# Kernel optimization log

Measured on AMD Instinct MI355X. Metric: run time of the kernel, lower is better.

## Reference

```python
import jax, jax.numpy as jnp
import numpy as np

N = 8192      # nodes
E = 16384     # query edges
D = 256       # node feature dim
NNZ = 262144  # overlap matrix nnz (avg degree 32)
P1, P2, P3 = 32, 32, 32


def _mlp(x, W1, b1, W2, b2):
    # Linear(1->p) -> ReLU -> Linear(p->1)
    return jax.nn.relu(x @ W1 + b1) @ W2 + b2


def setup_inputs() -> dict:
    key = jax.random.key(0)
    ks = jax.random.split(key, 16)
    inp = {
        "edges": jax.random.randint(ks[0], (E, 2), 0, N, dtype=jnp.int32),
        "row": jax.random.randint(ks[1], (NNZ,), 0, N, dtype=jnp.int32),
        "col": jax.random.randint(ks[2], (NNZ,), 0, N, dtype=jnp.int32),
        "values": jax.random.uniform(ks[3], (NNZ,), dtype=jnp.float32),
        "H": jax.random.normal(ks[4], (N, D), dtype=jnp.float32),
        # f_edge: 1 -> P1 -> 1
        "we1": jax.random.normal(ks[5], (1, P1), dtype=jnp.float32) * 0.5,
        "be1": jnp.zeros((P1,), jnp.float32),
        "we2": jax.random.normal(ks[6], (P1, 1), dtype=jnp.float32) * 0.5,
        "be2": jnp.zeros((1,), jnp.float32),
        # f_node: 1 -> P2 -> 1
        "wn1": jax.random.normal(ks[7], (1, P2), dtype=jnp.float32) * 0.5,
        "bn1": jnp.zeros((P2,), jnp.float32),
        "wn2": jax.random.normal(ks[8], (P2, 1), dtype=jnp.float32) * 0.5,
        "bn2": jnp.zeros((1,), jnp.float32),
        # psi_3: 1 -> P3 -> 1
        "wp1": jax.random.normal(ks[9], (1, P3), dtype=jnp.float32) * 0.5,
        "bp1": jnp.zeros((P3,), jnp.float32),
        "wp2": jax.random.normal(ks[10], (P3, 1), dtype=jnp.float32) * 0.5,
        "bp2": jnp.zeros((1,), jnp.float32),
        "alpha": jnp.zeros((2,), jnp.float32),
    }
    return inp


def reference(edges, row, col, values, H,
              we1, be1, we2, be2,
              wn1, bn1, wn2, bn2,
              wp1, bp1, wp2, bp2, alpha):
    src, dst = edges[:, 0], edges[:, 1]

    # --- BatchDotPred: sigmoid(<H[src], H[dst]>) ---
    h_link = jax.nn.sigmoid(jnp.einsum('ed,ed->e', H[src], H[dst]))[:, None]  # [E,1]

    # --- MultiHopAggregator ---
    edge_feat = _mlp(values[:, None], we1, be1, we2, be2)           # [NNZ,1]
    node_in = jax.ops.segment_sum(edge_feat, col, num_segments=N)  # [N,1] scatter_add over col
    struct = _mlp(node_in, wn1, bn1, wn2, bn2)[:, 0]                # [N]

    # dense overlap adjacency (coo.todense(), duplicates summed)
    adj = jnp.zeros((N, N), values.dtype).at[row, col].add(values)  # [N,N]

    # NOTE: faithful to source bug: both src and dst neighborhoods gather src rows
    sn = adj[src]                                                   # [E,N]
    agg = jnp.einsum('en,n->e', sn * sn, struct * struct)[:, None]  # [E,1]

    z_link = jax.nn.sigmoid(_mlp(agg, wp1, bp1, wp2, bp2))          # [E,1]

    a = jax.nn.softmax(alpha)
    y_hat = a[0] * z_link + a[1] * h_link + 1e-15
    return y_hat
```

## Files before the change

kernel.cpp:

```cpp
#include <hip/hip_runtime.h>
#include <math.h>

#define N_NODES 8192
#define D_DIM   256
#define E_EDGES 16384
#define NNZ_CNT 262144

#define NBLK 64
#define BTHR 1024
#define PER_BLK (NNZ_CNT / NBLK)

__device__ __forceinline__ float sigmoidf(float x) {
    return 1.0f / (1.0f + expf(-x));
}

__global__ void k_stage(const int* __restrict__ col,
                        const float* __restrict__ values,
                        const float* __restrict__ we1,
                        const float* __restrict__ be1,
                        const float* __restrict__ we2,
                        const float* __restrict__ be2,
                        float* __restrict__ partial) {
    __shared__ float bins[N_NODES];
    for (int j = threadIdx.x; j < N_NODES; j += BTHR) bins[j] = 0.0f;
    __syncthreads();
    int base = blockIdx.x * PER_BLK;
#pragma unroll
    for (int it = 0; it < PER_BLK / BTHR; ++it) {
        int k = base + it * BTHR + threadIdx.x;
        float v = values[k];
        int c = col[k];
        float f = be2[0];
#pragma unroll
        for (int j = 0; j < 32; ++j) {
            float t = fmaf(v, we1[j], be1[j]);
            t = t > 0.0f ? t : 0.0f;
            f = fmaf(t, we2[j], f);
        }
        atomicAdd(&bins[c], f);
    }
    __syncthreads();
    float* p = partial + (size_t)blockIdx.x * N_NODES;
    for (int j = threadIdx.x; j < N_NODES; j += BTHR) p[j] = bins[j];
}

__global__ void k_node(const float* __restrict__ partial,
                       const float* __restrict__ wn1,
                       const float* __restrict__ bn1,
                       const float* __restrict__ wn2,
                       const float* __restrict__ bn2,
                       float* __restrict__ struct2) {
    int i = blockIdx.x * blockDim.x + threadIdx.x;
    float x = 0.0f;
#pragma unroll 8
    for (int b = 0; b < NBLK; ++b) x += partial[(size_t)b * N_NODES + i];
    float u = bn2[0];
#pragma unroll
    for (int j = 0; j < 32; ++j) {
        float t = fmaf(x, wn1[j], bn1[j]);
        t = t > 0.0f ? t : 0.0f;
        u = fmaf(t, wn2[j], u);
    }
    struct2[i] = u * u;
}

__global__ void k_raccum(const int* __restrict__ row,
                         const int* __restrict__ col,
                         const float* __restrict__ values,
                         const float* __restrict__ struct2,
                         float* __restrict__ partial) {
    __shared__ float bins[N_NODES];
    for (int j = threadIdx.x; j < N_NODES; j += BTHR) bins[j] = 0.0f;
    __syncthreads();
    int base = blockIdx.x * PER_BLK;
#pragma unroll
    for (int it = 0; it < PER_BLK / BTHR; ++it) {
        int k = base + it * BTHR + threadIdx.x;
        float v = values[k];
        int r = row[k];
        int c = col[k];
        atomicAdd(&bins[r], v * v * struct2[c]);
    }
    __syncthreads();
    float* p = partial + (size_t)blockIdx.x * N_NODES;
    for (int j = threadIdx.x; j < N_NODES; j += BTHR) p[j] = bins[j];
}

__global__ void k_rreduce(const float* __restrict__ partial,
                          float* __restrict__ r) {
    int i = blockIdx.x * blockDim.x + threadIdx.x;
    float x = 0.0f;
#pragma unroll 8
    for (int b = 0; b < NBLK; ++b) x += partial[(size_t)b * N_NODES + i];
    r[i] = x;
}

__global__ void k_final(const int* __restrict__ edges,
                        const float* __restrict__ H,
                        const float* __restrict__ r,
                        const float* __restrict__ wp1,
                        const float* __restrict__ bp1,
                        const float* __restrict__ wp2,
                        const float* __restrict__ bp2,
                        const float* __restrict__ alpha,
                        float* __restrict__ out) {
    int e = blockIdx.x * (blockDim.x >> 6) + (threadIdx.x >> 6);
    int lane = threadIdx.x & 63;
    if (e >= E_EDGES) return;
    int src = edges[2 * e];
    int dst = edges[2 * e + 1];
    const float4* H4 = (const float4*)H;
    float4 a4 = H4[src * (D_DIM / 4) + lane];
    float4 b4 = H4[dst * (D_DIM / 4) + lane];
    float dot = a4.x * b4.x + a4.y * b4.y + a4.z * b4.z + a4.w * b4.w;
#pragma unroll
    for (int off = 32; off >= 1; off >>= 1)
        dot += __shfl_xor(dot, off, 64);
    if (lane == 0) {
        float h = sigmoidf(dot);
        float agg = r[src];
        float u = bp2[0];
#pragma unroll
        for (int j = 0; j < 32; ++j) {
            float t = fmaf(agg, wp1[j], bp1[j]);
            t = t > 0.0f ? t : 0.0f;
            u = fmaf(t, wp2[j], u);
        }
        float z = sigmoidf(u);
        float m = fmaxf(alpha[0], alpha[1]);
        float e0 = expf(alpha[0] - m);
        float e1 = expf(alpha[1] - m);
        float inv = 1.0f / (e0 + e1);
        out[e] = (e0 * inv) * z + (e1 * inv) * h + 1e-15f;
    }
}

extern "C" void kernel_launch(void* const* d_in, const int* in_sizes, int n_in,
                              void* d_out, int out_size, void* d_ws, size_t ws_size,
                              hipStream_t stream) {
    const int*   edges  = (const int*)d_in[0];
    const int*   row    = (const int*)d_in[1];
    const int*   col    = (const int*)d_in[2];
    const float* values = (const float*)d_in[3];
    const float* H      = (const float*)d_in[4];
    const float* we1    = (const float*)d_in[5];
    const float* be1    = (const float*)d_in[6];
    const float* we2    = (const float*)d_in[7];
    const float* be2    = (const float*)d_in[8];
    const float* wn1    = (const float*)d_in[9];
    const float* bn1    = (const float*)d_in[10];
    const float* wn2    = (const float*)d_in[11];
    const float* bn2    = (const float*)d_in[12];
    const float* wp1    = (const float*)d_in[13];
    const float* bp1    = (const float*)d_in[14];
    const float* wp2    = (const float*)d_in[15];
    const float* bp2    = (const float*)d_in[16];
    const float* alpha  = (const float*)d_in[17];
    float* out = (float*)d_out;

    float* ws_f    = (float*)d_ws;
    float* partial = ws_f;
    float* struct2 = ws_f + (size_t)NBLK * N_NODES;
    float* rbuf    = struct2 + N_NODES;

    k_stage<<<NBLK, BTHR, 0, stream>>>(col, values, we1, be1, we2, be2, partial);
    k_node<<<N_NODES / 1024, 1024, 0, stream>>>(partial, wn1, bn1, wn2, bn2, struct2);
    k_raccum<<<NBLK, BTHR, 0, stream>>>(row, col, values, struct2, partial);
    k_rreduce<<<N_NODES / 1024, 1024, 0, stream>>>(partial, rbuf);
    k_final<<<E_EDGES / 4, 256, 0, stream>>>(edges, H, rbuf, wp1, bp1, wp2, bp2, alpha, out);
}
```

Before: 130.8 us.

## Fuse five kernels into one cooperative kernel with grid syncs

Replaces the five separate launches (edge MLP scatter, node MLP, row accumulation, row reduce, final edge scoring) with a single cooperative kernel of 64 blocks that separates the phases with grid.sync. This removes per-launch overhead and inter-kernel gaps. The cost is that the final dot-product phase now runs on only 64 blocks (1024 waves) looping over edges instead of 4096 blocks, so it has less parallelism. It also adds the overhead of grid-wide barriers and a second partial buffer in the workspace.

```diff
diff --git a/kernel.cpp b/kernel.cpp
--- a/kernel.cpp
+++ b/kernel.cpp
@@ -1,5 +1,8 @@
 #include <hip/hip_runtime.h>
+#include <hip/hip_cooperative_groups.h>
 #include <math.h>
+
+namespace cg = cooperative_groups;
 
 #define N_NODES 8192
 #define D_DIM   256
@@ -14,158 +17,156 @@
     return 1.0f / (1.0f + expf(-x));
 }
 
-__global__ void k_stage(const int* __restrict__ col,
-                        const float* __restrict__ values,
-                        const float* __restrict__ we1,
-                        const float* __restrict__ be1,
-                        const float* __restrict__ we2,
-                        const float* __restrict__ be2,
-                        float* __restrict__ partial) {
+struct Params {
+    const int*   edges;
+    const int*   row;
+    const int*   col;
+    const float* values;
+    const float* H;
+    const float* we1; const float* be1; const float* we2; const float* be2;
+    const float* wn1; const float* bn1; const float* wn2; const float* bn2;
+    const float* wp1; const float* bp1; const float* wp2; const float* bp2;
+    const float* alpha;
+    float* out;
+    float* partA;
+    float* partB;
+    float* struct2;
+    float* rbuf;
+};
+
+__global__ __launch_bounds__(BTHR) void k_fused(Params p) {
+    cg::grid_group grid = cg::this_grid();
     __shared__ float bins[N_NODES];
-    for (int j = threadIdx.x; j < N_NODES; j += BTHR) bins[j] = 0.0f;
+    const int tid = threadIdx.x;
+    const int bid = blockIdx.x;
+    const int gid = bid * BTHR + tid;
+    const int base = bid * PER_BLK;
+
+    for (int j = tid; j < N_NODES; j += BTHR) bins[j] = 0.0f;
     __syncthreads();
-    int base = blockIdx.x * PER_BLK;
 #pragma unroll
     for (int it = 0; it < PER_BLK / BTHR; ++it) {
-        int k = base + it * BTHR + threadIdx.x;
-        float v = values[k];
-        int c = col[k];
-        float f = be2[0];
+        int k = base + it * BTHR + tid;
+        float v = p.values[k];
+        int c = p.col[k];
+        float f = p.be2[0];
 #pragma unroll
         for (int j = 0; j < 32; ++j) {
-            float t = fmaf(v, we1[j], be1[j]);
+            float t = fmaf(v, p.we1[j], p.be1[j]);
             t = t > 0.0f ? t : 0.0f;
-            f = fmaf(t, we2[j], f);
+            f = fmaf(t, p.we2[j], f);
         }
         atomicAdd(&bins[c], f);
     }
     __syncthreads();
-    float* p = partial + (size_t)blockIdx.x * N_NODES;
-    for (int j = threadIdx.x; j < N_NODES; j += BTHR) p[j] = bins[j];
-}
+    {
+        float* pa = p.partA + (size_t)bid * N_NODES;
+        for (int j = tid; j < N_NODES; j += BTHR) pa[j] = bins[j];
+    }
+    __threadfence();
+    grid.sync();
 
-__global__ void k_node(const float* __restrict__ partial,
-                       const float* __restrict__ wn1,
-                       const float* __restrict__ bn1,
-                       const float* __restrict__ wn2,
-                       const float* __restrict__ bn2,
-                       float* __restrict__ struct2) {
-    int i = blockIdx.x * blockDim.x + threadIdx.x;
-    float x = 0.0f;
+    if (gid < N_NODES) {
+        float x = 0.0f;
 #pragma unroll 8
-    for (int b = 0; b < NBLK; ++b) x += partial[(size_t)b * N_NODES + i];
-    float u = bn2[0];
+        for (int b = 0; b < NBLK; ++b) x += p.partA[(size_t)b * N_NODES + gid];
+        float u = p.bn2[0];
 #pragma unroll
-    for (int j = 0; j < 32; ++j) {
-        float t = fmaf(x, wn1[j], bn1[j]);
-        t = t > 0.0f ? t : 0.0f;
-        u = fmaf(t, wn2[j], u);
+        for (int j = 0; j < 32; ++j) {
+            float t = fmaf(x, p.wn1[j], p.bn1[j]);
+            t = t > 0.0f ? t : 0.0f;
+            u = fmaf(t, p.wn2[j], u);
+        }
+        p.struct2[gid] = u * u;
     }
-    struct2[i] = u * u;
-}
+    __threadfence();
+    grid.sync();
 
-__global__ void k_raccum(const int* __restrict__ row,
-                         const int* __restrict__ col,
-                         const float* __restrict__ values,
-                         const float* __restrict__ struct2,
-                         float* __restrict__ partial) {
-    __shared__ float bins[N_NODES];
-    for (int j = threadIdx.x; j < N_NODES; j += BTHR) bins[j] = 0.0f;
+    for (int j = tid; j < N_NODES; j += BTHR) bins[j] = 0.0f;
     __syncthreads();
-    int base = blockIdx.x * PER_BLK;
 #pragma unroll
     for (int it = 0; it < PER_BLK / BTHR; ++it) {
-        int k = base + it * BTHR + threadIdx.x;
-        float v = values[k];
-        int r = row[k];
-        int c = col[k];
-        atomicAdd(&bins[r], v * v * struct2[c]);
+        int k = base + it * BTHR + tid;
+        float v = p.values[k];
+        int r = p.row[k];
+        int c = p.col[k];
+        atomicAdd(&bins[r], v * v * p.struct2[c]);
     }
     __syncthreads();
-    float* p = partial + (size_t)blockIdx.x * N_NODES;
-    for (int j = threadIdx.x; j < N_NODES; j += BTHR) p[j] = bins[j];
-}
+    {
+        float* pb = p.partB + (size_t)bid * N_NODES;
+        for (int j = tid; j < N_NODES; j += BTHR) pb[j] = bins[j];
+    }
+    __threadfence();
+    grid.sync();
 
-__global__ void k_rreduce(const float* __restrict__ partial,
-                          float* __restrict__ r) {
-    int i = blockIdx.x * blockDim.x + threadIdx.x;
-    float x = 0.0f;
+    if (gid < N_NODES) {
+        float x = 0.0f;
 #pragma unroll 8
-    for (int b = 0; b < NBLK; ++b) x += partial[(size_t)b * N_NODES + i];
-    r[i] = x;
-}
+        for (int b = 0; b < NBLK; ++b) x += p.partB[(size_t)b * N_NODES + gid];
+        p.rbuf[gid] = x;
+    }
+    __threadfence();
+    grid.sync();
 
-__global__ void k_final(const int* __restrict__ edges,
-                        const float* __restrict__ H,
-                        const float* __restrict__ r,
-                        const float* __restrict__ wp1,
-                        const float* __restrict__ bp1,
-                        const float* __restrict__ wp2,
-                        const float* __restrict__ bp2,
-                        const float* __restrict__ alpha,
-                        float* __restrict__ out) {
-    int e = blockIdx.x * (blockDim.x >> 6) + (threadIdx.x >> 6);
-    int lane = threadIdx.x & 63;
-    if (e >= E_EDGES) return;
-    int src = edges[2 * e];
-    int dst = edges[2 * e + 1];
-    const float4* H4 = (const float4*)H;
-    float4 a4 = H4[src * (D_DIM / 4) + lane];
-    float4 b4 = H4[dst * (D_DIM / 4) + lane];
-    float dot = a4.x * b4.x + a4.y * b4.y + a4.z * b4.z + a4.w * b4.w;
+    const int wave  = gid >> 6;
+    const int lane  = tid & 63;
+    const int nwave = (NBLK * BTHR) >> 6;
+    const float4* H4 = (const float4*)p.H;
+    for (int e = wave; e < E_EDGES; e += nwave) {
+        int src = p.edges[2 * e];
+        int dst = p.edges[2 * e + 1];
+        float4 a4 = H4[src * (D_DIM / 4) + lane];
+        float4 b4 = H4[dst * (D_DIM / 4) + lane];
+        float dot = a4.x * b4.x + a4.y * b4.y + a4.z * b4.z + a4.w * b4.w;
 #pragma unroll
-    for (int off = 32; off >= 1; off >>= 1)
-        dot += __shfl_xor(dot, off, 64);
-    if (lane == 0) {
-        float h = sigmoidf(dot);
-        float agg = r[src];
-        float u = bp2[0];
+        for (int off = 32; off >= 1; off >>= 1)
+            dot += __shfl_xor(dot, off, 64);
+        if (lane == 0) {
+            float h = sigmoidf(dot);
+            float agg = p.rbuf[src];
+            float u = p.bp2[0];
 #pragma unroll
-        for (int j = 0; j < 32; ++j) {
-            float t = fmaf(agg, wp1[j], bp1[j]);
-            t = t > 0.0f ? t : 0.0f;
-            u = fmaf(t, wp2[j], u);
+            for (int j = 0; j < 32; ++j) {
+                float t = fmaf(agg, p.wp1[j], p.bp1[j]);
+                t = t > 0.0f ? t : 0.0f;
+                u = fmaf(t, p.wp2[j], u);
+            }
+            float z = sigmoidf(u);
+            float m = fmaxf(p.alpha[0], p.alpha[1]);
+            float e0 = expf(p.alpha[0] - m);
+            float e1 = expf(p.alpha[1] - m);
+            float inv = 1.0f / (e0 + e1);
+            p.out[e] = (e0 * inv) * z + (e1 * inv) * h + 1e-15f;
         }
-        float z = sigmoidf(u);
-        float m = fmaxf(alpha[0], alpha[1]);
-        float e0 = expf(alpha[0] - m);
-        float e1 = expf(alpha[1] - m);
-        float inv = 1.0f / (e0 + e1);
-        out[e] = (e0 * inv) * z + (e1 * inv) * h + 1e-15f;
     }
 }
 
 extern "C" void kernel_launch(void* const* d_in, const int* in_sizes, int n_in,
                               void* d_out, int out_size, void* d_ws, size_t ws_size,
                               hipStream_t stream) {
-    const int*   edges  = (const int*)d_in[0];
-    const int*   row    = (const int*)d_in[1];
-    const int*   col    = (const int*)d_in[2];
-    const float* values = (const float*)d_in[3];
-    const float* H      = (const float*)d_in[4];
-    const float* we1    = (const float*)d_in[5];
-    const float* be1    = (const float*)d_in[6];
-    const float* we2    = (const float*)d_in[7];
-    const float* be2    = (const float*)d_in[8];
-    const float* wn1    = (const float*)d_in[9];
-    const float* bn1    = (const float*)d_in[10];
-    const float* wn2    = (const float*)d_in[11];
-    const float* bn2    = (const float*)d_in[12];
-    const float* wp1    = (const float*)d_in[13];
-    const float* bp1    = (const float*)d_in[14];
-    const float* wp2    = (const float*)d_in[15];
-    const float* bp2    = (const float*)d_in[16];
-    const float* alpha  = (const float*)d_in[17];
-    float* out = (float*)d_out;
+    Params prm;
+    prm.edges  = (const int*)d_in[0];
+    prm.row    = (const int*)d_in[1];
+    prm.col    = (const int*)d_in[2];
+    prm.values = (const float*)d_in[3];
+    prm.H      = (const float*)d_in[4];
+    prm.we1 = (const float*)d_in[5];  prm.be1 = (const float*)d_in[6];
+    prm.we2 = (const float*)d_in[7];  prm.be2 = (const float*)d_in[8];
+    prm.wn1 = (const float*)d_in[9];  prm.bn1 = (const float*)d_in[10];
+    prm.wn2 = (const float*)d_in[11]; prm.bn2 = (const float*)d_in[12];
+    prm.wp1 = (const float*)d_in[13]; prm.bp1 = (const float*)d_in[14];
+    prm.wp2 = (const float*)d_in[15]; prm.bp2 = (const float*)d_in[16];
+    prm.alpha = (const float*)d_in[17];
+    prm.out = (float*)d_out;
 
-    float* ws_f    = (float*)d_ws;
-    float* partial = ws_f;
-    float* struct2 = ws_f + (size_t)NBLK * N_NODES;
-    float* rbuf    = struct2 + N_NODES;
+    float* ws_f = (float*)d_ws;
+    prm.partA   = ws_f;
+    prm.partB   = ws_f + (size_t)NBLK * N_NODES;
+    prm.struct2 = ws_f + (size_t)2 * NBLK * N_NODES;
+    prm.rbuf    = prm.struct2 + N_NODES;
 
-    k_stage<<<NBLK, BTHR, 0, stream>>>(col, values, we1, be1, we2, be2, partial);
-    k_node<<<N_NODES / 1024, 1024, 0, stream>>>(partial, wn1, bn1, wn2, bn2, struct2);
-    k_raccum<<<NBLK, BTHR, 0, stream>>>(row, col, values, struct2, partial);
-    k_rreduce<<<N_NODES / 1024, 1024, 0, stream>>>(partial, rbuf);
-    k_final<<<E_EDGES / 4, 256, 0, stream>>>(edges, H, rbuf, wp1, bp1, wp2, bp2, alpha, out);
+    void* args[] = { &prm };
+    hipLaunchCooperativeKernel((void*)k_fused, dim3(NBLK), dim3(BTHR),
+                               args, 0, stream);
 }
```

New measurement: 321.5 us. 2.46x slower.
